# Performance work log

Hardware: AMD Instinct MI355X
Metric: run time of the kernel (lower is better)

The kernel has to match this reference:

```python
import jax, jax.numpy as jnp
import numpy as np

IN_SZ, KZ, H, B, T = 8, 3, 512, 64, 1024
N_AUX = 7


def setup_inputs() -> dict:
    key = jax.random.key(0)
    ks = jax.random.split(key, 32)
    stdv = 1.0 / np.sqrt(H)
    u = lambda k, shape: jax.random.uniform(k, shape, jnp.float32, -stdv, stdv)
    inp = {}
    inp['Y'] = jax.random.normal(ks[0], (B, IN_SZ, T), jnp.float32)
    for i in range(N_AUX):
        inp[f'x{i+1}'] = jax.random.normal(ks[1 + i], (B, KZ, T), jnp.float32)
    # main gate params
    inp['W_i'] = u(ks[8], (IN_SZ, H)); inp['U_i'] = u(ks[9], (H, H)); inp['b_i'] = u(ks[10], (H,))
    inp['W_f'] = u(ks[11], (IN_SZ, H)); inp['U_f'] = u(ks[12], (H, H)); inp['b_f'] = u(ks[13], (H,))
    inp['W_c'] = u(ks[14], (IN_SZ, H)); inp['U_c'] = u(ks[15], (H, H)); inp['b_c'] = u(ks[16], (H,))
    inp['W_o'] = u(ks[17], (IN_SZ, H)); inp['U_o'] = u(ks[18], (H, H)); inp['b_o'] = u(ks[19], (H,))
    # stacked aux params: index k over the 7 auxiliary inputs
    inp['W_i_x'] = u(ks[20], (N_AUX, KZ, H)); inp['U_i_x'] = u(ks[21], (N_AUX, H, H)); inp['b_i_x'] = u(ks[22], (N_AUX, H))
    inp['W_c_x'] = u(ks[23], (N_AUX, KZ, H)); inp['U_c_x'] = u(ks[24], (N_AUX, H, H)); inp['b_c_x'] = u(ks[25], (N_AUX, H))
    inp['W_a'] = u(ks[26], (H, H)); inp['b_a'] = u(ks[27], (H,))
    return inp


def reference(Y, x1, x2, x3, x4, x5, x6, x7,
              W_i, U_i, b_i, W_f, U_f, b_f, W_c, U_c, b_c, W_o, U_o, b_o,
              W_i_x, U_i_x, b_i_x, W_c_x, U_c_x, b_c_x, W_a, b_a):
    bs = Y.shape[0]
    hid = U_i.shape[0]
    # NOTE: original code (faithfully reproduced) feeds x2 into the input gates
    # of aux channels 3..7, while the candidate cell states use x3..x7.
    xi = jnp.stack([x1, x2, x2, x2, x2, x2, x2])          # [7,B,3,T]
    xc = jnp.stack([x1, x2, x3, x4, x5, x6, x7])          # [7,B,3,T]
    Y_t = jnp.transpose(Y, (2, 0, 1))                     # [T,B,in]
    xi_t = jnp.transpose(xi, (3, 0, 1, 2))                # [T,7,B,3]
    xc_t = jnp.transpose(xc, (3, 0, 1, 2))                # [T,7,B,3]

    def step(carry, inp):
        h, c = carry
        Yt, xit, xct = inp
        i_t = jax.nn.sigmoid(Yt @ W_i + h @ U_i + b_i)
        f_t = jax.nn.sigmoid(Yt @ W_f + h @ U_f + b_f)
        Ct = jnp.tanh(Yt @ W_c + h @ U_c + b_c)
        o_t = jax.nn.sigmoid(Yt @ W_o + h @ U_o + b_o)
        i_x = jax.nn.sigmoid(jnp.einsum('kbc,kch->kbh', xit, W_i_x)
                             + jnp.einsum('bh,khg->kbg', h, U_i_x)
                             + b_i_x[:, None, :])          # [7,B,H]
        C_x = jnp.tanh(jnp.einsum('kbc,kch->kbh', xct, W_c_x)
                       + jnp.einsum('bh,khg->kbg', h, U_c_x)
                       + b_c_x[:, None, :])                # [7,B,H]
        l = jnp.concatenate([(Ct * i_t)[None], C_x * i_x], axis=0)  # [8,B,H]
        u = jnp.tanh(jnp.einsum('kbh,hg->kbg', l, W_a) * c + b_a)   # [8,B,H]
        alpha = jax.nn.softmax(u, axis=0)
        L = jnp.sum(alpha * l, axis=0)
        c_new = f_t * c + L
        h_new = o_t * jnp.tanh(c_new)
        return (h_new, c_new), h_new

    h0 = jnp.zeros((bs, hid), Y.dtype)
    c0 = jnp.zeros((bs, hid), Y.dtype)
    (h_T, _), hs = jax.lax.scan(step, (h0, c0), (Y_t, xi_t, xc_t))
    hidden_seq = jnp.transpose(hs, (1, 0, 2))             # [B,T,H]
    return h_T, hidden_seq
```

## Files before the change

### kernel.cpp

```cpp
#include <hip/hip_runtime.h>


typedef _Float16 f16;
typedef _Float16 f16x8 __attribute__((ext_vector_type(8)));
typedef float    f32x4 __attribute__((ext_vector_type(4)));
typedef unsigned int       u32;
typedef unsigned long long u64;
typedef unsigned short     u16;

#define DI static __device__ __forceinline__

constexpr int B_   = 64;
constexpr int H_   = 512;
constexpr int T_   = 1024;
constexpr int NWG  = 208;
constexpr int NTHR = 512;
constexpr int NA_WG = 144;

constexpr size_t MAT_ELE = (size_t)16 * 32 * 64 * 8;

constexpr int OFF_W    = 0;
constexpr int OFF_SMX  = 65536;
constexpr int OFF_UF   = 81920;
constexpr int OFF_CLDS = 98304;
constexpr int OFF_SBA  = 100352;
constexpr int OFF_RED  = 131072;
constexpr int OFF_SINI = 147456;
constexpr int OFF_SINC = 149504;
constexpr int OFF_SWI  = 151552;
constexpr int OFF_SWC  = 152576;
constexpr int OFF_SBI  = 153600;
constexpr int OFF_SBC  = 153728;
constexpr int OFF_STG  = 153856;
constexpr int POOL_SZ  = 162048;

__device__ __align__(64) u16 g_hflag[64];
__device__ __align__(64) u16 g_lflag[144];
__device__ u32 g_hp[2][B_ * H_];
__device__ u32 g_lp[2][8 * B_ * H_];
__device__ u64 g_fo[2][B_ * H_];
__device__ f16 g_blob1[19 * MAT_ELE];
__device__ f16 g_blob2[19 * MAT_ELE];

struct P {
  const float* Y;
  const float* x[7];
  const float *W_i, *U_i, *b_i, *W_f, *U_f, *b_f;
  const float *W_c, *U_c, *b_c, *W_o, *U_o, *b_o;
  const float *W_i_x, *U_i_x, *b_i_x, *W_c_x, *U_c_x, *b_c_x;
  const float *W_a, *b_a;
  float* out;
};

DI f32x4 mfma16(f16x8 a, f16x8 b, f32x4 c) {
  return __builtin_amdgcn_mfma_f32_16x16x32_f16(a, b, c, 0, 0, 0);
}
DI float sigmoidf_(float x) { return 1.0f / (1.0f + expf(-x)); }

DI u32 lda32(const u32* p) {
  return __hip_atomic_load(p, __ATOMIC_RELAXED, __HIP_MEMORY_SCOPE_AGENT);
}
DI void sta32(u32* p, u32 v) {
  __hip_atomic_store(p, v, __ATOMIC_RELAXED, __HIP_MEMORY_SCOPE_AGENT);
}
DI u64 lda64(const void* p) {
  return __hip_atomic_load((const u64*)p, __ATOMIC_RELAXED, __HIP_MEMORY_SCOPE_AGENT);
}
DI void sta64(void* p, u64 v) {
  __hip_atomic_store((u64*)p, v, __ATOMIC_RELAXED, __HIP_MEMORY_SCOPE_AGENT);
}
DI void sta16(u16* p, u16 v) {
  __hip_atomic_store(p, v, __ATOMIC_RELAXED, __HIP_MEMORY_SCOPE_AGENT);
}
DI u16 f16bits(f16 h) { return __builtin_bit_cast(u16, h); }
DI f16  bitsf16(u16 b) { return __builtin_bit_cast(f16, b); }

DI bool flags4_ge(u64 v, u32 tgt) {
  return ((u32)(v & 0xffffu) >= tgt) && ((u32)((v >> 16) & 0xffffu) >= tgt) &&
         ((u32)((v >> 32) & 0xffffu) >= tgt) && ((u32)(v >> 48) >= tgt);
}

__global__ void __launch_bounds__(256) prep_kernel(P p) {
  const int gid = blockIdx.x * blockDim.x + threadIdx.x;
  const int nth = gridDim.x * blockDim.x;
  if (gid < 32) ((u32*)g_hflag)[gid] = 0u;
  if (gid < 72) ((u32*)g_lflag)[gid] = 0u;
  for (int i = gid; i < 2 * B_ * H_; i += nth) ((u32*)g_hp)[i] = 0u;

  const int lane = threadIdx.x & 63;
  const int wvg  = gid >> 6;
  const int nwv  = nth >> 6;
  for (int tile = wvg; tile < 19 * 16 * 32; tile += nwv) {
    const int mat = tile / (16 * 32);
    const int rem = tile % (16 * 32);
    const int kt = rem >> 5, nt = rem & 31;
    const float* src;
    if      (mat == 0)  src = p.U_i;
    else if (mat <  8)  src = p.U_i_x + (size_t)(mat - 1) * H_ * H_;
    else if (mat == 8)  src = p.U_f;
    else if (mat == 9)  src = p.U_c;
    else if (mat < 17)  src = p.U_c_x + (size_t)(mat - 10) * H_ * H_;
    else if (mat == 17) src = p.U_o;
    else                src = p.W_a;
    const int k0 = kt * 32 + (lane >> 4) * 8;
    const int n  = nt * 16 + (lane & 15);
    f16x8 hv, lv;
#pragma unroll
    for (int j = 0; j < 8; ++j) {
      float v  = src[(size_t)(k0 + j) * H_ + n];
      f16   hh = (f16)v;
      hv[j] = hh;
      lv[j] = (f16)((v - (float)hh) * 2048.0f);
    }
    size_t off = (size_t)mat * MAT_ELE + ((size_t)(kt * 32 + nt) * 64 + lane) * 8;
    *(f16x8*)(g_blob1 + off) = hv;
    *(f16x8*)(g_blob2 + off) = lv;
  }
}

__global__ void __launch_bounds__(NTHR, 2) lstm_main(P p) {
  const int wg   = blockIdx.x;
  const int tid  = threadIdx.x;
  const int lane = tid & 63;
  const int wv   = tid >> 6;
  const int quad = lane >> 4;
  const int l15  = lane & 15;

  __shared__ __align__(16) char pool[POOL_SZ];
  float* sInI = (float*)(pool + OFF_SINI);
  float* sInC = (float*)(pool + OFF_SINC);
  float* sWI  = (float*)(pool + OFF_SWI);
  float* sWC  = (float*)(pool + OFF_SWC);
  float* sbI  = (float*)(pool + OFF_SBI);
  float* sbC  = (float*)(pool + OFF_SBC);
  float* sba  = (float*)(pool + OFF_SBA);
  float* cl_  = (float*)(pool + OFF_CLDS);
  float* redf = (float*)(pool + OFF_RED);
  float* uf   = (float*)(pool + OFF_UF);
  u32*   stg  = (u32*)(pool + OFF_STG);

  const bool isA = (wg < NA_WG);

  int kap = 0, C0A = 0, KI = 8, nt0 = 0, ktA = 0;
  const float* inI = p.Y;
  const float* inC = p.Y;
  int R0B = 0, C0B = 0;

  if (isA) {
    kap = wg >> 4;
    C0A = (wg & 15) * 32;
    nt0 = C0A >> 4;
    ktA = wg & 15;
    KI  = (kap == 0 || kap == 8) ? 8 : 3;
    int matI, matC;
    const float *WIs, *bIs, *WCs, *bCs;
    if (kap == 0)      { WIs = p.W_i; bIs = p.b_i; WCs = p.W_c; bCs = p.b_c; matI = 0; matC = 9; }
    else if (kap == 8) { WIs = p.W_f; bIs = p.b_f; WCs = p.W_o; bCs = p.b_o; matI = 8; matC = 17; }
    else {
      WIs = p.W_i_x + (size_t)(kap - 1) * 3 * H_;
      bIs = p.b_i_x + (size_t)(kap - 1) * H_;
      WCs = p.W_c_x + (size_t)(kap - 1) * 3 * H_;
      bCs = p.b_c_x + (size_t)(kap - 1) * H_;
      inI = (kap == 1) ? p.x[0] : p.x[1];
      inC = p.x[kap - 1];
      matI = kap; matC = 9 + kap;
    }
    for (int idx = tid; idx < KI * 32; idx += NTHR) {
      int i = idx >> 5, c = idx & 31;
      sWI[i * 32 + c] = WIs[(size_t)i * H_ + C0A + c];
      sWC[i * 32 + c] = WCs[(size_t)i * H_ + C0A + c];
    }
    if (tid < 32) { sbI[tid] = bIs[C0A + tid]; sbC[tid] = bCs[C0A + tid]; }
    for (int c = tid; c < 8192; c += NTHR) {
      int frag = c >> 6, ln = c & 63;
      int half = frag & 1, nn = (frag >> 1) & 1, kt = (frag >> 2) & 15, ms = frag >> 6;
      int mat = ms ? matC : matI;
      size_t so = (size_t)mat * MAT_ELE + ((size_t)(kt * 32 + nt0 + nn) * 64 + ln) * 8;
      *(f16x8*)(pool + OFF_W + (size_t)frag * 1024 + ln * 16) =
          *(const f16x8*)((half ? g_blob2 : g_blob1) + so);
    }
  } else {
    int w2 = wg - NA_WG;
    R0B = (w2 >> 4) * 16;
    C0B = (w2 & 15) * 32;
    nt0 = C0B >> 4;
    if (tid < 32) sba[tid] = p.b_a[C0B + tid];
    for (int idx = tid; idx < 512; idx += NTHR) cl_[idx] = 0.0f;
    for (int c = tid; c < 4096; c += NTHR) {
      int frag = c >> 6, ln = c & 63;
      int half = frag & 1, nn = (frag >> 1) & 1, kt = frag >> 2;
      size_t so = (size_t)18 * MAT_ELE + ((size_t)(kt * 32 + nt0 + nn) * 64 + ln) * 8;
      *(f16x8*)(pool + OFF_W + (size_t)frag * 1024 + ln * 16) =
          *(const f16x8*)((half ? g_blob2 : g_blob1) + so);
    }
  }
  __syncthreads();

  for (int t = 0; t < T_; ++t) {
    if (isA) {
      for (int idx = tid; idx < 64 * KI; idx += NTHR) {
        int b = idx / KI, i = idx % KI;
        sInI[b * 8 + i] = inI[((size_t)b * KI + i) * T_ + t];
        sInC[b * 8 + i] = inC[((size_t)b * KI + i) * T_ + t];
      }
      if (wv == 0) {
        const u32 tgt = (u32)t;
        int spin = 0;
        for (;;) {
          bool ok = true;
          if (lane < 16) ok = flags4_ge(lda64((const u64*)g_hflag + lane), tgt);
          if (__all(ok)) break;
          if (spin > 2) __builtin_amdgcn_s_sleep(4);
          else          __builtin_amdgcn_s_sleep(1);
          ++spin;
        }
      }
      __syncthreads();

      const int mh2 = wv >> 1, kh = wv & 1;
      const int ktBase = kh * 8;
      const u64* hF = (const u64*)g_hp[(t + 1) & 1] +
                      ((size_t)(mh2 * 16 + ktBase) * 4) * 64 + lane;

      u64 raw[2][4][4];
#pragma unroll
      for (int k2 = 0; k2 < 4; ++k2) {
#pragma unroll
        for (int j = 0; j < 4; ++j)
          raw[0][k2][j] = lda64(hF + (size_t)(k2 * 4 + j) * 64);
      }
      f32x4 acc[2][2][2] = {};
      __builtin_amdgcn_s_setprio(1);
      for (int g = 0; g < 2; ++g) {
        if (g == 0) {
#pragma unroll
          for (int k2 = 0; k2 < 4; ++k2) {
#pragma unroll
            for (int j = 0; j < 4; ++j)
              raw[1][k2][j] = lda64(hF + (size_t)((4 + k2) * 4 + j) * 64);
          }
        }
#pragma unroll
        for (int k2 = 0; k2 < 4; ++k2) {
          int kt = ktBase + g * 4 + k2;
          union { u64 q[4]; u32 w[8]; } r;
          r.q[0] = raw[g][k2][0]; r.q[1] = raw[g][k2][1];
          r.q[2] = raw[g][k2][2]; r.q[3] = raw[g][k2][3];
          union { f16x8 v; u16 s[8]; } ah, al;
#pragma unroll
          for (int j = 0; j < 8; ++j) {
            ah.s[j] = (u16)(r.w[j] & 0xffffu);
            al.s[j] = (u16)(r.w[j] >> 16);
          }
#pragma unroll
          for (int mat = 0; mat < 2; ++mat)
#pragma unroll
            for (int nn = 0; nn < 2; ++nn) {
              int f = ((mat * 16 + kt) * 2 + nn) * 2;
              f16x8 w1 = *(const f16x8*)(pool + OFF_W + (size_t)f * 1024 + lane * 16);
              f16x8 w2 = *(const f16x8*)(pool + OFF_W + (size_t)(f + 1) * 1024 + lane * 16);
              acc[mat][nn][0] = mfma16(ah.v, w1, acc[mat][nn][0]);
              acc[mat][nn][1] = mfma16(ah.v, w2, acc[mat][nn][1]);
              acc[mat][nn][1] = mfma16(al.v, w1, acc[mat][nn][1]);
            }
        }
      }
      __builtin_amdgcn_s_setprio(0);

      if (kh == 1) {
#pragma unroll
        for (int mat = 0; mat < 2; ++mat)
#pragma unroll
          for (int nn = 0; nn < 2; ++nn) {
            f32x4 comb = acc[mat][nn][0] + acc[mat][nn][1] * (1.0f / 2048.0f);
            *(f32x4*)(redf + mh2 * 1024 + ((mat * 2 + nn) * 64 + lane) * 4) = comb;
          }
      }
      __syncthreads();

      if (kh == 0) {
#pragma unroll
        for (int nn = 0; nn < 2; ++nn) {
          f32x4 tot[2];
#pragma unroll
          for (int mat = 0; mat < 2; ++mat) {
            f32x4 oth = *(const f32x4*)(redf + mh2 * 1024 + ((mat * 2 + nn) * 64 + lane) * 4);
            tot[mat] = acc[mat][nn][0] + acc[mat][nn][1] * (1.0f / 2048.0f) + oth;
          }
#pragma unroll
          for (int r4 = 0; r4 < 4; ++r4) {
            int brow = mh2 * 16 + quad * 4 + r4;
            int cc = nn * 16 + l15;
            float pre0 = tot[0][r4] + sbI[cc];
            float pre1 = tot[1][r4] + sbC[cc];
            for (int i = 0; i < KI; ++i) {
              pre0 += sInI[brow * 8 + i] * sWI[i * 32 + cc];
              pre1 += sInC[brow * 8 + i] * sWC[i * 32 + cc];
            }
            if (kap == 8) {
              float fg = sigmoidf_(pre0);
              float og = sigmoidf_(pre1);
              u64 v = (u64)__builtin_bit_cast(u32, fg) |
                      ((u64)__builtin_bit_cast(u32, og) << 32);
              sta64(&g_fo[t & 1][(size_t)brow * H_ + C0A + cc], v);
            } else {
              float lv = sigmoidf_(pre0) * tanhf(pre1);
              f16 hi = (f16)lv;
              f16 lo = (f16)((lv - (float)hi) * 2048.0f);
              u32 pw = (u32)f16bits(hi) | ((u32)f16bits(lo) << 16);
              int quadl = cc >> 3, jl = (cc & 7) >> 1, half = cc & 1;
              stg[(((mh2 * 4 + jl) * 64) + quadl * 16 + quad * 4 + r4) * 2 + half] = pw;
            }
          }
        }
      }
      __syncthreads();
      if (kap != 8) {
        const u64* stg64 = (const u64*)(pool + OFF_STG);
        u64* dst = (u64*)g_lp[t & 1];
#pragma unroll
        for (int e = 0; e < 2; ++e) {
          int el = tid + e * 512;
          int m2 = el >> 8, rem = el & 255;
          sta64(dst + ((size_t)(kap * 4 + m2) * 16 + ktA) * 256 + rem, stg64[el]);
        }
      }
      __syncthreads();
      if (tid == 0) sta16(&g_lflag[wg], (u16)(t + 1));

    } else {
      if (wv == 0) {
        const u32 tgt = (u32)(t + 1);
        int spin = 0;
        for (;;) {
          bool ok = true;
          if (lane < 36) ok = flags4_ge(lda64((const u64*)g_lflag + lane), tgt);
          if (__all(ok)) break;
          if (spin > 2) __builtin_amdgcn_s_sleep(4);
          else          __builtin_amdgcn_s_sleep(1);
          ++spin;
        }
      }
      __syncthreads();

      u64 foPre = lda64(&g_fo[t & 1][(size_t)(R0B + (tid >> 5)) * H_ + C0B + (tid & 31)]);

      const int chP = wv >> 1, kh = wv & 1;
      const int ktBase = kh * 8;
      const int mh2B = R0B >> 4;
      const u64* lF = (const u64*)g_lp[t & 1];
      const int smxkt = C0B >> 5;

      const u64* lb[2];
#pragma unroll
      for (int ch = 0; ch < 2; ++ch)
        lb[ch] = lF + ((((size_t)(chP * 2 + ch) * 4 + mh2B) * 16 + ktBase) * 4) * 64 + lane;

      u64 raw[2][4][2][4];
#pragma unroll
      for (int k2 = 0; k2 < 4; ++k2)
#pragma unroll
        for (int ch = 0; ch < 2; ++ch) {
#pragma unroll
          for (int j = 0; j < 4; ++j)
            raw[0][k2][ch][j] = lda64(lb[ch] + (size_t)(k2 * 4 + j) * 64);
        }
      f32x4 acc[2][2][2] = {};
      __builtin_amdgcn_s_setprio(1);
      for (int g = 0; g < 2; ++g) {
        if (g == 0) {
#pragma unroll
          for (int k2 = 0; k2 < 4; ++k2)
#pragma unroll
            for (int ch = 0; ch < 2; ++ch) {
#pragma unroll
              for (int j = 0; j < 4; ++j)
                raw[1][k2][ch][j] = lda64(lb[ch] + (size_t)((4 + k2) * 4 + j) * 64);
            }
        }
#pragma unroll
        for (int k2 = 0; k2 < 4; ++k2) {
          int kt = ktBase + g * 4 + k2;
#pragma unroll
          for (int ch = 0; ch < 2; ++ch) {
            union { u64 q[4]; u32 w[8]; } r;
            r.q[0] = raw[g][k2][ch][0]; r.q[1] = raw[g][k2][ch][1];
            r.q[2] = raw[g][k2][ch][2]; r.q[3] = raw[g][k2][ch][3];
            if (kt == smxkt) {
              u32* d = (u32*)(pool + OFF_SMX +
                       (((size_t)(chP * 2 + ch) * 16 + l15) * 32 + quad * 8) * 4);
              *(uint4*)d       = make_uint4(r.w[0], r.w[1], r.w[2], r.w[3]);
              *(uint4*)(d + 4) = make_uint4(r.w[4], r.w[5], r.w[6], r.w[7]);
            }
            union { f16x8 v; u16 s[8]; } ah, al;
#pragma unroll
            for (int j = 0; j < 8; ++j) {
              ah.s[j] = (u16)(r.w[j] & 0xffffu);
              al.s[j] = (u16)(r.w[j] >> 16);
            }
#pragma unroll
            for (int nn = 0; nn < 2; ++nn) {
              int f = (kt * 2 + nn) * 2;
              f16x8 w1 = *(const f16x8*)(pool + OFF_W + (size_t)f * 1024 + lane * 16);
              f16x8 w2 = *(const f16x8*)(pool + OFF_W + (size_t)(f + 1) * 1024 + lane * 16);
              acc[ch][nn][0] = mfma16(ah.v, w1, acc[ch][nn][0]);
              acc[ch][nn][1] = mfma16(ah.v, w2, acc[ch][nn][1]);
              acc[ch][nn][1] = mfma16(al.v, w1, acc[ch][nn][1]);
            }
          }
        }
      }
      __builtin_amdgcn_s_setprio(0);

      if (kh == 1) {
#pragma unroll
        for (int ch = 0; ch < 2; ++ch)
#pragma unroll
          for (int nn = 0; nn < 2; ++nn) {
            f32x4 comb = acc[ch][nn][0] + acc[ch][nn][1] * (1.0f / 2048.0f);
            *(f32x4*)(redf + chP * 1024 + ((ch * 2 + nn) * 64 + lane) * 4) = comb;
          }
      }
      __syncthreads();
      if (kh == 0) {
#pragma unroll
        for (int ch = 0; ch < 2; ++ch)
#pragma unroll
          for (int nn = 0; nn < 2; ++nn) {
            f32x4 oth = *(const f32x4*)(redf + chP * 1024 + ((ch * 2 + nn) * 64 + lane) * 4);
            f32x4 dot = acc[ch][nn][0] + acc[ch][nn][1] * (1.0f / 2048.0f) + oth;
#pragma unroll
            for (int r4 = 0; r4 < 4; ++r4) {
              int bl = quad * 4 + r4;
              int cc = nn * 16 + l15;
              float uv = tanhf(dot[r4] * cl_[bl * 32 + cc] + sba[cc]);
              uf[(chP * 2 + ch) * 512 + bl * 32 + cc] = uv;
            }
          }
      }
      __syncthreads();

      {
        int bl = tid >> 5, cc = tid & 31;
        int bg = R0B + bl, cgl = C0B + cc;
        float uv[8], um = -1e30f;
#pragma unroll
        for (int k = 0; k < 8; ++k) { uv[k] = uf[k * 512 + tid]; um = fmaxf(um, uv[k]); }
        float e[8], s = 0.0f;
#pragma unroll
        for (int k = 0; k < 8; ++k) { e[k] = expf(uv[k] - um); s += e[k]; }
        float inv = 1.0f / s;
        float L = 0.0f;
#pragma unroll
        for (int k = 0; k < 8; ++k) {
          u32 pw = *(const u32*)(pool + OFF_SMX + ((size_t)k * 512 + tid) * 4);
          float lvv = (float)bitsf16((u16)(pw & 0xffffu)) +
                      (float)bitsf16((u16)(pw >> 16)) * (1.0f / 2048.0f);
          L += e[k] * inv * lvv;
        }
        float fg = __builtin_bit_cast(float, (u32)(foPre & 0xffffffffu));
        float og = __builtin_bit_cast(float, (u32)(foPre >> 32));
        float co = cl_[bl * 32 + cc];
        float cn = fg * co + L;
        float hn = og * tanhf(cn);
        cl_[bl * 32 + cc] = cn;
        f16 hh = (f16)hn;
        f16 hl = (f16)((hn - (float)hh) * 2048.0f);
        {
          int quadl = cc >> 3, jl = (cc & 7) >> 1, half = cc & 1;
          stg[((jl * 64) + quadl * 16 + bl) * 2 + half] =
              (u32)f16bits(hh) | ((u32)f16bits(hl) << 16);
        }
        p.out[(size_t)B_ * H_ + ((size_t)bg * T_ + t) * H_ + cgl] = hn;
        if (t == T_ - 1) p.out[(size_t)bg * H_ + cgl] = hn;
      }
      __syncthreads();
      if (tid < 256) {
        const u64* stg64 = (const u64*)(pool + OFF_STG);
        sta64((u64*)g_hp[t & 1] + ((size_t)(R0B >> 4) * 16 + (C0B >> 5)) * 256 + tid,
              stg64[tid]);
      }
      __syncthreads();
      if (tid == 0) sta16(&g_hflag[wg - NA_WG], (u16)(t + 1));
    }
  }
}

extern "C" void kernel_launch(void* const* d_in, const int* in_sizes, int n_in,
                              void* d_out, int out_size, void* d_ws, size_t ws_size,
                              hipStream_t stream) {
  (void)in_sizes; (void)n_in; (void)out_size; (void)d_ws; (void)ws_size;

  P p;
  p.Y = (const float*)d_in[0];
  for (int i = 0; i < 7; ++i) p.x[i] = (const float*)d_in[1 + i];
  p.W_i   = (const float*)d_in[8];  p.U_i   = (const float*)d_in[9];  p.b_i   = (const float*)d_in[10];
  p.W_f   = (const float*)d_in[11]; p.U_f   = (const float*)d_in[12]; p.b_f   = (const float*)d_in[13];
  p.W_c   = (const float*)d_in[14]; p.U_c   = (const float*)d_in[15]; p.b_c   = (const float*)d_in[16];
  p.W_o   = (const float*)d_in[17]; p.U_o   = (const float*)d_in[18]; p.b_o   = (const float*)d_in[19];
  p.W_i_x = (const float*)d_in[20]; p.U_i_x = (const float*)d_in[21]; p.b_i_x = (const float*)d_in[22];
  p.W_c_x = (const float*)d_in[23]; p.U_c_x = (const float*)d_in[24]; p.b_c_x = (const float*)d_in[25];
  p.W_a   = (const float*)d_in[26]; p.b_a   = (const float*)d_in[27];
  p.out   = (float*)d_out;

  prep_kernel<<<dim3(256), dim3(256), 0, stream>>>(p);

  void* kargs[] = { (void*)&p };
  hipError_t err = hipLaunchCooperativeKernel((void*)lstm_main, dim3(NWG), dim3(NTHR),
                                              kargs, 0, stream);
  if (err != hipSuccess) {
    lstm_main<<<dim3(NWG), dim3(NTHR), 0, stream>>>(p);
  }
}
```

Before: 24.99 ms.

## Halve B-stage workgroups, widening each to 64 columns with streamed low weights

The attention/cell-update stage now runs on 32 workgroups instead of 64, and each covers 16 rows by 64 columns. This halves the number of flags the A-stage polls and reduces per-step synchronisation fan-in. The low-half W_a fragments no longer fit in LDS, so they are double-buffered from global memory during the MFMA loop. The global output stores are moved after the h-flag release so they sit off the critical path. The trade is twice the MFMA and elementwise work per B workgroup, plus extra global weight traffic every step.

After: 48.19 ms. +92.9%, slower.

```diff
diff --git a/kernel.cpp b/kernel.cpp
--- a/kernel.cpp
+++ b/kernel.cpp
@@ -13,17 +13,16 @@
 constexpr int B_   = 64;
 constexpr int H_   = 512;
 constexpr int T_   = 1024;
-constexpr int NWG  = 208;
 constexpr int NTHR = 512;
 constexpr int NA_WG = 144;
+constexpr int NB_WG = 32;
+constexpr int NWG  = NA_WG + NB_WG;
 
 constexpr size_t MAT_ELE = (size_t)16 * 32 * 64 * 8;
 
 constexpr int OFF_W    = 0;
 constexpr int OFF_SMX  = 65536;
-constexpr int OFF_UF   = 81920;
-constexpr int OFF_CLDS = 98304;
-constexpr int OFF_SBA  = 100352;
+constexpr int OFF_UF   = 98304;
 constexpr int OFF_RED  = 131072;
 constexpr int OFF_SINI = 147456;
 constexpr int OFF_SINC = 149504;
@@ -31,10 +30,12 @@
 constexpr int OFF_SWC  = 152576;
 constexpr int OFF_SBI  = 153600;
 constexpr int OFF_SBC  = 153728;
+constexpr int OFF_CLDS = 147456;
+constexpr int OFF_SBA  = 151552;
 constexpr int OFF_STG  = 153856;
 constexpr int POOL_SZ  = 162048;
 
-__device__ __align__(64) u16 g_hflag[64];
+__device__ __align__(64) u16 g_hflag[32];
 __device__ __align__(64) u16 g_lflag[144];
 __device__ u32 g_hp[2][B_ * H_];
 __device__ u32 g_lp[2][8 * B_ * H_];
@@ -80,10 +81,14 @@
          ((u32)((v >> 32) & 0xffffu) >= tgt) && ((u32)(v >> 48) >= tgt);
 }
 
+DI f16x8 ldw(const f16* base, int kt, int nt, int lane) {
+  return *(const f16x8*)(base + (((size_t)(kt * 32 + nt) * 64 + lane) * 8));
+}
+
 __global__ void __launch_bounds__(256) prep_kernel(P p) {
   const int gid = blockIdx.x * blockDim.x + threadIdx.x;
   const int nth = gridDim.x * blockDim.x;
-  if (gid < 32) ((u32*)g_hflag)[gid] = 0u;
+  if (gid < 16) ((u32*)g_hflag)[gid] = 0u;
   if (gid < 72) ((u32*)g_lflag)[gid] = 0u;
   for (int i = gid; i < 2 * B_ * H_; i += nth) ((u32*)g_hp)[i] = 0u;
 
@@ -181,19 +186,19 @@
     }
   } else {
     int w2 = wg - NA_WG;
-    R0B = (w2 >> 4) * 16;
-    C0B = (w2 & 15) * 32;
+    R0B = (w2 >> 3) * 16;
+    C0B = (w2 & 7) * 64;
     nt0 = C0B >> 4;
-    if (tid < 32) sba[tid] = p.b_a[C0B + tid];
-    for (int idx = tid; idx < 512; idx += NTHR) cl_[idx] = 0.0f;
+    if (tid < 64) sba[tid] = p.b_a[C0B + tid];
+    for (int idx = tid; idx < 1024; idx += NTHR) cl_[idx] = 0.0f;
     for (int c = tid; c < 4096; c += NTHR) {
       int frag = c >> 6, ln = c & 63;
-      int half = frag & 1, nn = (frag >> 1) & 1, kt = frag >> 2;
+      int kt = frag >> 2, nn = frag & 3;
       size_t so = (size_t)18 * MAT_ELE + ((size_t)(kt * 32 + nt0 + nn) * 64 + ln) * 8;
-      *(f16x8*)(pool + OFF_W + (size_t)frag * 1024 + ln * 16) =
-          *(const f16x8*)((half ? g_blob2 : g_blob1) + so);
+      *(f16x8*)(pool + OFF_W + (size_t)frag * 1024 + ln * 16) = *(const f16x8*)(g_blob1 + so);
     }
   }
+  const f16* loA = g_blob2 + (size_t)18 * MAT_ELE;
   __syncthreads();
 
   for (int t = 0; t < T_; ++t) {
@@ -208,7 +213,7 @@
         int spin = 0;
         for (;;) {
           bool ok = true;
-          if (lane < 16) ok = flags4_ge(lda64((const u64*)g_hflag + lane), tgt);
+          if (lane < 8) ok = flags4_ge(lda64((const u64*)g_hflag + lane), tgt);
           if (__all(ok)) break;
           if (spin > 2) __builtin_amdgcn_s_sleep(4);
           else          __builtin_amdgcn_s_sleep(1);
@@ -343,13 +348,14 @@
       }
       __syncthreads();
 
-      u64 foPre = lda64(&g_fo[t & 1][(size_t)(R0B + (tid >> 5)) * H_ + C0B + (tid & 31)]);
+      u64 foPre0 = lda64(&g_fo[t & 1][(size_t)(R0B + (tid >> 6)) * H_ + C0B + (tid & 63)]);
+      u64 foPre1 = lda64(&g_fo[t & 1][(size_t)(R0B + 8 + (tid >> 6)) * H_ + C0B + (tid & 63)]);
 
       const int chP = wv >> 1, kh = wv & 1;
       const int ktBase = kh * 8;
       const int mh2B = R0B >> 4;
       const u64* lF = (const u64*)g_lp[t & 1];
-      const int smxkt = C0B >> 5;
+      const int ktp = C0B >> 5;
 
       const u64* lb[2];
 #pragma unroll
@@ -365,7 +371,10 @@
           for (int j = 0; j < 4; ++j)
             raw[0][k2][ch][j] = lda64(lb[ch] + (size_t)(k2 * 4 + j) * 64);
         }
-      f32x4 acc[2][2][2] = {};
+      f32x4 acc[2][4][2] = {};
+      f16x8 w2b[2][4];
+#pragma unroll
+      for (int nn = 0; nn < 4; ++nn) w2b[0][nn] = ldw(loA, ktBase, nt0 + nn, lane);
       __builtin_amdgcn_s_setprio(1);
       for (int g = 0; g < 2; ++g) {
         if (g == 0) {
@@ -380,15 +389,21 @@
         }
 #pragma unroll
         for (int k2 = 0; k2 < 4; ++k2) {
-          int kt = ktBase + g * 4 + k2;
+          const int jj8 = g * 4 + k2;
+          const int kt = ktBase + jj8;
+          if (jj8 < 7) {
+#pragma unroll
+            for (int nn = 0; nn < 4; ++nn)
+              w2b[(jj8 + 1) & 1][nn] = ldw(loA, kt + 1, nt0 + nn, lane);
+          }
 #pragma unroll
           for (int ch = 0; ch < 2; ++ch) {
             union { u64 q[4]; u32 w[8]; } r;
             r.q[0] = raw[g][k2][ch][0]; r.q[1] = raw[g][k2][ch][1];
             r.q[2] = raw[g][k2][ch][2]; r.q[3] = raw[g][k2][ch][3];
-            if (kt == smxkt) {
-              u32* d = (u32*)(pool + OFF_SMX +
-                       (((size_t)(chP * 2 + ch) * 16 + l15) * 32 + quad * 8) * 4);
+            if (kt == ktp || kt == ktp + 1) {
+              u32* d = (u32*)(pool + OFF_SMX) +
+                       ((size_t)(chP * 2 + ch) * 16 + l15) * 64 + (kt - ktp) * 32 + quad * 8;
               *(uint4*)d       = make_uint4(r.w[0], r.w[1], r.w[2], r.w[3]);
               *(uint4*)(d + 4) = make_uint4(r.w[4], r.w[5], r.w[6], r.w[7]);
             }
@@ -399,12 +414,11 @@
               al.s[j] = (u16)(r.w[j] >> 16);
             }
 #pragma unroll
-            for (int nn = 0; nn < 2; ++nn) {
-              int f = (kt * 2 + nn) * 2;
+            for (int nn = 0; nn < 4; ++nn) {
+              int f = kt * 4 + nn;
               f16x8 w1 = *(const f16x8*)(pool + OFF_W + (size_t)f * 1024 + lane * 16);
-              f16x8 w2 = *(const f16x8*)(pool + OFF_W + (size_t)(f + 1) * 1024 + lane * 16);
               acc[ch][nn][0] = mfma16(ah.v, w1, acc[ch][nn][0]);
-              acc[ch][nn][1] = mfma16(ah.v, w2, acc[ch][nn][1]);
+              acc[ch][nn][1] = mfma16(ah.v, w2b[jj8 & 1][nn], acc[ch][nn][1]);
               acc[ch][nn][1] = mfma16(al.v, w1, acc[ch][nn][1]);
             }
           }
@@ -412,76 +426,84 @@
       }
       __builtin_amdgcn_s_setprio(0);
 
-      if (kh == 1) {
-#pragma unroll
-        for (int ch = 0; ch < 2; ++ch)
-#pragma unroll
-          for (int nn = 0; nn < 2; ++nn) {
-            f32x4 comb = acc[ch][nn][0] + acc[ch][nn][1] * (1.0f / 2048.0f);
-            *(f32x4*)(redf + chP * 1024 + ((ch * 2 + nn) * 64 + lane) * 4) = comb;
-          }
-      }
-      __syncthreads();
-      if (kh == 0) {
-#pragma unroll
-        for (int ch = 0; ch < 2; ++ch)
-#pragma unroll
-          for (int nn = 0; nn < 2; ++nn) {
-            f32x4 oth = *(const f32x4*)(redf + chP * 1024 + ((ch * 2 + nn) * 64 + lane) * 4);
-            f32x4 dot = acc[ch][nn][0] + acc[ch][nn][1] * (1.0f / 2048.0f) + oth;
+#pragma unroll
+      for (int rch = 0; rch < 2; ++rch) {
+        if (kh == 1) {
+#pragma unroll
+          for (int nn = 0; nn < 4; ++nn)
+            *(f32x4*)(redf + chP * 1024 + (nn * 64 + lane) * 4) =
+                acc[rch][nn][0] + acc[rch][nn][1] * (1.0f / 2048.0f);
+        }
+        __syncthreads();
+        if (kh == 0) {
+#pragma unroll
+          for (int nn = 0; nn < 4; ++nn) {
+            f32x4 dot = acc[rch][nn][0] + acc[rch][nn][1] * (1.0f / 2048.0f) +
+                        *(const f32x4*)(redf + chP * 1024 + (nn * 64 + lane) * 4);
 #pragma unroll
             for (int r4 = 0; r4 < 4; ++r4) {
               int bl = quad * 4 + r4;
               int cc = nn * 16 + l15;
-              float uv = tanhf(dot[r4] * cl_[bl * 32 + cc] + sba[cc]);
-              uf[(chP * 2 + ch) * 512 + bl * 32 + cc] = uv;
-            }
-          }
-      }
-      __syncthreads();
-
-      {
-        int bl = tid >> 5, cc = tid & 31;
+              float uv = tanhf(dot[r4] * cl_[bl * 64 + cc] + sba[cc]);
+              uf[(size_t)(chP * 2 + rch) * 1024 + bl * 64 + cc] = uv;
+            }
+          }
+        }
+        __syncthreads();
+      }
+
+      float hnOut[2];
+      int bgOut[2], cglOut[2];
+#pragma unroll
+      for (int e = 0; e < 2; ++e) {
+        int idx = tid + e * 512;
+        int bl = idx >> 6, cc = idx & 63;
         int bg = R0B + bl, cgl = C0B + cc;
         float uv[8], um = -1e30f;
 #pragma unroll
-        for (int k = 0; k < 8; ++k) { uv[k] = uf[k * 512 + tid]; um = fmaxf(um, uv[k]); }
-        float e[8], s = 0.0f;
-#pragma unroll
-        for (int k = 0; k < 8; ++k) { e[k] = expf(uv[k] - um); s += e[k]; }
+        for (int k = 0; k < 8; ++k) {
+          uv[k] = uf[(size_t)k * 1024 + bl * 64 + cc];
+          um = fmaxf(um, uv[k]);
+        }
+        float ee[8], s = 0.0f;
+#pragma unroll
+        for (int k = 0; k < 8; ++k) { ee[k] = expf(uv[k] - um); s += ee[k]; }
         float inv = 1.0f / s;
         float L = 0.0f;
 #pragma unroll
         for (int k = 0; k < 8; ++k) {
-          u32 pw = *(const u32*)(pool + OFF_SMX + ((size_t)k * 512 + tid) * 4);
+          u32 pw = *((const u32*)(pool + OFF_SMX) + (size_t)k * 1024 + bl * 64 + cc);
           float lvv = (float)bitsf16((u16)(pw & 0xffffu)) +
                       (float)bitsf16((u16)(pw >> 16)) * (1.0f / 2048.0f);
-          L += e[k] * inv * lvv;
-        }
-        float fg = __builtin_bit_cast(float, (u32)(foPre & 0xffffffffu));
-        float og = __builtin_bit_cast(float, (u32)(foPre >> 32));
-        float co = cl_[bl * 32 + cc];
+          L += ee[k] * inv * lvv;
+        }
+        u64 fo = e ? foPre1 : foPre0;
+        float fg = __builtin_bit_cast(float, (u32)(fo & 0xffffffffu));
+        float og = __builtin_bit_cast(float, (u32)(fo >> 32));
+        float co = cl_[bl * 64 + cc];
         float cn = fg * co + L;
         float hn = og * tanhf(cn);
-        cl_[bl * 32 + cc] = cn;
+        cl_[bl * 64 + cc] = cn;
         f16 hh = (f16)hn;
         f16 hl = (f16)((hn - (float)hh) * 2048.0f);
-        {
-          int quadl = cc >> 3, jl = (cc & 7) >> 1, half = cc & 1;
-          stg[((jl * 64) + quadl * 16 + bl) * 2 + half] =
-              (u32)f16bits(hh) | ((u32)f16bits(hl) << 16);
-        }
-        p.out[(size_t)B_ * H_ + ((size_t)bg * T_ + t) * H_ + cgl] = hn;
-        if (t == T_ - 1) p.out[(size_t)bg * H_ + cgl] = hn;
-      }
-      __syncthreads();
-      if (tid < 256) {
+        stg[((cc >> 5) * 256 + ((cc & 7) >> 1) * 64 + ((cc & 31) >> 3) * 16 + bl) * 2 +
+            (cc & 1)] = (u32)f16bits(hh) | ((u32)f16bits(hl) << 16);
+        hnOut[e] = hn; bgOut[e] = bg; cglOut[e] = cgl;
+      }
+      __syncthreads();
+      {
         const u64* stg64 = (const u64*)(pool + OFF_STG);
-        sta64((u64*)g_hp[t & 1] + ((size_t)(R0B >> 4) * 16 + (C0B >> 5)) * 256 + tid,
+        sta64((u64*)g_hp[t & 1] +
+                  ((size_t)(mh2B * 16 + ktp + (tid >> 8))) * 256 + (tid & 255),
               stg64[tid]);
       }
       __syncthreads();
       if (tid == 0) sta16(&g_hflag[wg - NA_WG], (u16)(t + 1));
+#pragma unroll
+      for (int e = 0; e < 2; ++e) {
+        p.out[(size_t)B_ * H_ + ((size_t)bgOut[e] * T_ + t) * H_ + cglOut[e]] = hnOut[e];
+        if (t == T_ - 1) p.out[(size_t)bgOut[e] * H_ + cglOut[e]] = hnOut[e];
+      }
     }
   }
 }
```
